# Performance work log

Hardware: AMD Instinct MI355X
Metric: run time of the kernel (lower is better)

## Reference

```python
import jax, jax.numpy as jnp
import numpy as np

N_NODES = 50000
N_EDGES = 800000
N_FEAT = 128
DIM = 64
N_GRAPHS = 512


def setup_inputs() -> dict:
    key = jax.random.key(0)
    k1, k2, k3, k4, k5, k6 = jax.random.split(key, 6)
    x = jax.random.normal(k1, (N_NODES, N_FEAT), dtype=jnp.float32)
    edge_index = jax.random.randint(k2, (2, N_EDGES), 0, N_NODES, dtype=jnp.int64)
    batch = jnp.sort(jax.random.randint(k3, (N_NODES,), 0, N_GRAPHS, dtype=jnp.int64))
    W1 = jax.random.normal(k4, (N_FEAT, DIM), dtype=jnp.float32) * 0.05
    W2 = jax.random.normal(k5, (DIM, DIM), dtype=jnp.float32) * 0.05
    Wfc = jax.random.normal(k6, (DIM, 1), dtype=jnp.float32) * 0.05
    return {"x": x, "edge_index": edge_index, "batch": batch,
            "W1": W1, "W2": W2, "Wfc": Wfc}


def _gcn_conv(h, src, dst, W):
    # GCNConv(normalize=False, bias=False): linear transform then scatter-add
    # over edges: out[dst] += (h @ W)[src]
    h = jnp.einsum('nf,fd->nd', h, W)
    return jax.ops.segment_sum(h[src], dst, num_segments=N_NODES)


def reference(x, edge_index, batch, W1, W2, Wfc):
    src, dst = edge_index[0], edge_index[1]
    h = jax.nn.relu(_gcn_conv(x, src, dst, W1))          # [N, DIM]
    h = _gcn_conv(h, src, dst, W2)                        # [N, DIM]
    # global_mean_pool over graph ids
    counts = jax.ops.segment_sum(jnp.ones((N_NODES,), h.dtype), batch,
                                 num_segments=N_GRAPHS)   # [G]
    pooled = jax.ops.segment_sum(h, batch, num_segments=N_GRAPHS)
    pooled = pooled / jnp.maximum(counts, 1.0)[:, None]   # [G, DIM]
    return jax.nn.sigmoid(pooled @ Wfc)                   # [G, 1]
```

## Files before the change

kernel.cpp:

```cpp
#include <hip/hip_runtime.h>
#include <cmath>

#define N_NODES 50000
#define N_EDGES 800000
#define N_FEAT 128
#define DIM 64
#define N_GRAPHS 512
#define GGRID ((N_NODES + 63) / 64)
#define NBKT GGRID
#define BH_BLK 256
#define EPB (N_EDGES / BH_BLK)
#define BKT_CAP 2048

__device__ __forceinline__ unsigned short f2bf(float f) {
  union { float f; unsigned int u; } v; v.f = f;
  return (unsigned short)((v.u + 0x7FFFu + ((v.u >> 16) & 1u)) >> 16);
}
__device__ __forceinline__ float bf2f(unsigned short u) {
  union { unsigned int u; float f; } v; v.u = (unsigned int)u << 16;
  return v.f;
}

template<int K>
__device__ __forceinline__ void gemm_body_bf(const float* __restrict__ A,
                                             const float* __restrict__ W,
                                             unsigned short* __restrict__ out,
                                             int M, int row0, int tid,
                                             float* sX, float* sW) {
  const int tx = tid & 15, ty = tid >> 4;
  const int q = tid & 7, r0 = tid >> 3;
  float acc[4][4] = {};

  for (int kb = 0; kb < K; kb += 32) {
    __syncthreads();
    if ((kb & 63) == 0) {
#pragma unroll
      for (int i = 0; i < 16; i++)
        sW[i * 256 + tid] = W[kb * 64 + i * 256 + tid];
    }
#pragma unroll
    for (int rr = 0; rr < 64; rr += 32) {
      int r = r0 + rr;
      int gr = row0 + r;
      float4 v = make_float4(0.f, 0.f, 0.f, 0.f);
      if (gr < M) v = *(const float4*)&A[(size_t)gr * K + kb + q * 4];
      *(float4*)&sX[r * 36 + q * 4] = v;
    }
    __syncthreads();

    const int kw = kb & 63;
#pragma unroll 4
    for (int k = 0; k < 32; k += 4) {
      float4 wv[4];
#pragma unroll
      for (int kk = 0; kk < 4; kk++)
        wv[kk] = *(const float4*)&sW[(kw + k + kk) * 64 + tx * 4];
#pragma unroll
      for (int r = 0; r < 4; r++) {
        float4 xv = *(const float4*)&sX[(ty * 4 + r) * 36 + k];
        const float xs[4] = {xv.x, xv.y, xv.z, xv.w};
#pragma unroll
        for (int kk = 0; kk < 4; kk++) {
          acc[r][0] += xs[kk] * wv[kk].x;
          acc[r][1] += xs[kk] * wv[kk].y;
          acc[r][2] += xs[kk] * wv[kk].z;
          acc[r][3] += xs[kk] * wv[kk].w;
        }
      }
    }
  }

#pragma unroll
  for (int r = 0; r < 4; r++) {
    int gr = row0 + ty * 4 + r;
    if (gr < M) {
      ushort4 u;
      u.x = f2bf(acc[r][0]); u.y = f2bf(acc[r][1]);
      u.z = f2bf(acc[r][2]); u.w = f2bf(acc[r][3]);
      *(ushort4*)&out[(size_t)gr * 64 + tx * 4] = u;
    }
  }
}

__global__ __launch_bounds__(256) void fused_main(
    const float* __restrict__ x, const float* __restrict__ W1,
    unsigned short* __restrict__ h1, const int* __restrict__ src,
    const int* __restrict__ dst, int* __restrict__ gcur,
    unsigned int* __restrict__ ebuf, const float* __restrict__ W2,
    const float* __restrict__ Wfc, float* __restrict__ w2fc) {
  __shared__ float sX[64 * 36];
  __shared__ float sW[64 * 64];
  const int tid = threadIdx.x;
  if (blockIdx.x < BH_BLK) {
    int* lh = (int*)sX;
    int* lbase = (int*)sW;
    int* lcur = lbase + NBKT;
    for (int i = tid; i < NBKT; i += 256) { lh[i] = 0; lcur[i] = 0; }
    __syncthreads();
    const int base = blockIdx.x * EPB;
    for (int j = tid; j < EPB; j += 256)
      atomicAdd(&lh[dst[base + j] >> 6], 1);
    __syncthreads();
    for (int i = tid; i < NBKT; i += 256) {
      int n = lh[i];
      lbase[i] = (n > 0) ? i * BKT_CAP + atomicAdd(&gcur[i], n) : 0;
    }
    __syncthreads();
    for (int j = tid; j < EPB; j += 256) {
      int e = base + j;
      int d = dst[e];
      int b = d >> 6;
      int pos = atomicAdd(&lcur[b], 1);
      unsigned int gpos = (unsigned int)(lbase[b] + pos);
      if (gpos < (unsigned int)((b + 1) * BKT_CAP))
        ebuf[gpos] = ((unsigned int)src[e] << 6) | (unsigned int)(d & 63);
    }
  } else if (blockIdx.x == BH_BLK) {
    int k = tid;
    if (k < 64) {
      float s = 0.f;
#pragma unroll 8
      for (int j = 0; j < 64; j++) s += W2[k * 64 + j] * Wfc[j];
      w2fc[k] = s;
    }
  } else {
    gemm_body_bf<N_FEAT>(x, W1, h1, N_NODES, (blockIdx.x - BH_BLK - 1) * 64,
                         tid, sX, sW);
  }
}

__global__ __launch_bounds__(1024, 8) void gather_z_fused(
    const unsigned short* __restrict__ h1,
    const unsigned int* __restrict__ ebuf,
    const int* __restrict__ gcur,
    const float* __restrict__ w2fc,
    float* __restrict__ z) {
  __shared__ unsigned int eL[BKT_CAP];
  __shared__ int colL[BKT_CAP];
  __shared__ int lstart[64];
  __shared__ int lcur[64];
  __shared__ float sw[64];
  const int tid = threadIdx.x;
  const int b = blockIdx.x;
  const int p0 = b * BKT_CAP;
  int cnt = gcur[b];
  if (cnt > BKT_CAP) cnt = BKT_CAP;

  if (tid < 64) { lstart[tid] = 0; sw[tid] = w2fc[tid]; }
  __syncthreads();
  for (int i = tid; i < cnt; i += 1024) {
    unsigned int u = ebuf[p0 + i];
    eL[i] = u;
    atomicAdd(&lstart[u & 63], 1);
  }
  __syncthreads();
  if (tid < 64) {
    int v = lstart[tid], s = v;
#pragma unroll
    for (int off = 1; off < 64; off <<= 1) {
      int t = __shfl_up(s, off, 64);
      if (tid >= off) s += t;
    }
    lstart[tid] = s - v;
    lcur[tid] = s - v;
  }
  __syncthreads();
  for (int i = tid; i < cnt; i += 1024) {
    unsigned int u = eL[i];
    int pos = atomicAdd(&lcur[u & 63], 1);
    colL[pos] = (int)(u >> 6);
  }
  __syncthreads();

  const int lane = tid & 63, w = tid >> 6;
  const int eo = lane >> 4, qfo = (lane & 15) << 2;
#pragma unroll
  for (int ni = 0; ni < 4; ni++) {
    const int r = ni * 16 + w;
    const int i1 = lcur[r];
    int i = lstart[r];
    float4 acc = make_float4(0.f, 0.f, 0.f, 0.f);
    for (; i + 16 <= i1; i += 16) {
      int s0 = colL[i + eo];
      int s1 = colL[i + 4 + eo];
      int s2 = colL[i + 8 + eo];
      int s3 = colL[i + 12 + eo];
      ushort4 u0 = *(const ushort4*)&h1[(size_t)s0 * 64 + qfo];
      ushort4 u1 = *(const ushort4*)&h1[(size_t)s1 * 64 + qfo];
      ushort4 u2 = *(const ushort4*)&h1[(size_t)s2 * 64 + qfo];
      ushort4 u3 = *(const ushort4*)&h1[(size_t)s3 * 64 + qfo];
      acc.x += (bf2f(u0.x) + bf2f(u1.x)) + (bf2f(u2.x) + bf2f(u3.x));
      acc.y += (bf2f(u0.y) + bf2f(u1.y)) + (bf2f(u2.y) + bf2f(u3.y));
      acc.z += (bf2f(u0.z) + bf2f(u1.z)) + (bf2f(u2.z) + bf2f(u3.z));
      acc.w += (bf2f(u0.w) + bf2f(u1.w)) + (bf2f(u2.w) + bf2f(u3.w));
    }
    for (; i + 4 <= i1; i += 4) {
      int s = colL[i + eo];
      ushort4 u = *(const ushort4*)&h1[(size_t)s * 64 + qfo];
      acc.x += bf2f(u.x); acc.y += bf2f(u.y);
      acc.z += bf2f(u.z); acc.w += bf2f(u.w);
    }
    if (eo < i1 - i) {
      int s = colL[i + eo];
      ushort4 u = *(const ushort4*)&h1[(size_t)s * 64 + qfo];
      acc.x += bf2f(u.x); acc.y += bf2f(u.y);
      acc.z += bf2f(u.z); acc.w += bf2f(u.w);
    }
#pragma unroll
    for (int m = 16; m <= 32; m <<= 1) {
      acc.x += __shfl_xor(acc.x, m, 64);
      acc.y += __shfl_xor(acc.y, m, 64);
      acc.z += __shfl_xor(acc.z, m, 64);
      acc.w += __shfl_xor(acc.w, m, 64);
    }
    float p = fmaxf(acc.x, 0.f) * sw[qfo] + fmaxf(acc.y, 0.f) * sw[qfo + 1] +
              fmaxf(acc.z, 0.f) * sw[qfo + 2] + fmaxf(acc.w, 0.f) * sw[qfo + 3];
#pragma unroll
    for (int m = 1; m <= 8; m <<= 1) p += __shfl_xor(p, m, 64);
    int node = b * 64 + r;
    if (lane == 0 && node < N_NODES) z[node] = p;
  }
}

__global__ __launch_bounds__(256) void graph_pool(const float* __restrict__ z,
                                                  const unsigned int* __restrict__ ebuf,
                                                  const int* __restrict__ gcur,
                                                  const int* __restrict__ batch,
                                                  float* __restrict__ out) {
  __shared__ float sacc[4];
  int g = blockIdx.x;
  int tid = threadIdx.x, lane = tid & 63, w = tid >> 6;

  int lo = 0, hi = N_NODES;
  while (lo < hi) { int mid = (lo + hi) >> 1; if (batch[mid] < g) lo = mid + 1; else hi = mid; }
  const int start = lo;
  hi = N_NODES;
  while (lo < hi) { int mid = (lo + hi) >> 1; if (batch[mid] < g + 1) lo = mid + 1; else hi = mid; }
  const int end = lo;

  float s = 0.f;
  if (end > start) {
    const int b0 = start >> 6, b1 = ((end - 1) >> 6) + 1;
    for (int b = b0; b < b1; b++) {
      int bc = gcur[b];
      if (bc > BKT_CAP) bc = BKT_CAP;
      const int q0 = b * BKT_CAP, q1 = q0 + bc;
      const int base = b << 6;
      for (int i = q0 + tid; i < q1; i += 256) {
        unsigned int u = ebuf[i];
        int d = base + (int)(u & 63);
        if (d >= start && d < end) s += z[u >> 6];
      }
    }
  }
#pragma unroll
  for (int off = 32; off; off >>= 1) s += __shfl_down(s, off, 64);
  if (lane == 0) sacc[w] = s;
  __syncthreads();
  if (tid == 0) {
    float v = sacc[0] + sacc[1] + sacc[2] + sacc[3];
    v /= fmaxf((float)(end - start), 1.f);
    out[g] = 1.f / (1.f + expf(-v));
  }
}

extern "C" void kernel_launch(void* const* d_in, const int* in_sizes, int n_in,
                              void* d_out, int out_size, void* d_ws, size_t ws_size,
                              hipStream_t stream) {
  const float* x     = (const float*)d_in[0];
  const int*   ei    = (const int*)d_in[1];
  const int*   batch = (const int*)d_in[2];
  const float* W1    = (const float*)d_in[3];
  const float* W2    = (const float*)d_in[4];
  const float* Wfc   = (const float*)d_in[5];
  float*       out   = (float*)d_out;

  const int* src = ei;
  const int* dst = ei + N_EDGES;

  char* ws = (char*)d_ws;
  unsigned short* h1 = (unsigned short*)(ws);
  float* z    = (float*)(ws + (size_t)N_NODES * DIM * 2);
  float* w2fc = z + N_NODES;
  int*   gcur = (int*)(w2fc + 64);
  unsigned int* ebuf = (unsigned int*)(gcur + 800);

  hipMemsetAsync(gcur, 0, NBKT * sizeof(int), stream);
  fused_main<<<BH_BLK + 1 + GGRID, 256, 0, stream>>>(x, W1, h1, src, dst,
                                                     gcur, ebuf, W2, Wfc, w2fc);

  gather_z_fused<<<NBKT, 1024, 0, stream>>>(h1, ebuf, gcur, w2fc, z);

  graph_pool<<<N_GRAPHS, 256, 0, stream>>>(z, ebuf, gcur, batch, out);
}
```

Before: 138.6 us.

## Compute first GEMM with split-bf16 MFMA and fold memset into a W1 split kernel

Replaces the scalar FP32 shared-memory GEMM for x@W1 with bf16 MFMA 16x16x32 instructions. It keeps near-fp32 accuracy by splitting each operand into high and low bf16 halves and doing three MFMAs per tile. W1 is pre-split and transposed by a new small init kernel, which also zeroes the bucket counters and so replaces the memset. The x tile is converted to bf16 hi/lo on load into an XOR-swizzled LDS layout. The cost is an extra launch, more LDS (32KB per block), and B operands read directly from global memory.

```diff
diff --git a/kernel.cpp b/kernel.cpp
--- a/kernel.cpp
+++ b/kernel.cpp
@@ -12,6 +12,9 @@
 #define EPB (N_EDGES / BH_BLK)
 #define BKT_CAP 2048
 
+typedef short short8 __attribute__((ext_vector_type(8)));
+typedef float floatx4 __attribute__((ext_vector_type(4)));
+
 __device__ __forceinline__ unsigned short f2bf(float f) {
   union { float f; unsigned int u; } v; v.f = f;
   return (unsigned short)((v.u + 0x7FFFu + ((v.u >> 16) & 1u)) >> 16);
@@ -21,80 +24,99 @@
   return v.f;
 }
 
-template<int K>
-__device__ __forceinline__ void gemm_body_bf(const float* __restrict__ A,
-                                             const float* __restrict__ W,
-                                             unsigned short* __restrict__ out,
-                                             int M, int row0, int tid,
-                                             float* sX, float* sW) {
-  const int tx = tid & 15, ty = tid >> 4;
-  const int q = tid & 7, r0 = tid >> 3;
-  float acc[4][4] = {};
-
-  for (int kb = 0; kb < K; kb += 32) {
-    __syncthreads();
-    if ((kb & 63) == 0) {
-#pragma unroll
-      for (int i = 0; i < 16; i++)
-        sW[i * 256 + tid] = W[kb * 64 + i * 256 + tid];
-    }
-#pragma unroll
-    for (int rr = 0; rr < 64; rr += 32) {
-      int r = r0 + rr;
-      int gr = row0 + r;
-      float4 v = make_float4(0.f, 0.f, 0.f, 0.f);
-      if (gr < M) v = *(const float4*)&A[(size_t)gr * K + kb + q * 4];
-      *(float4*)&sX[r * 36 + q * 4] = v;
-    }
-    __syncthreads();
-
-    const int kw = kb & 63;
-#pragma unroll 4
-    for (int k = 0; k < 32; k += 4) {
-      float4 wv[4];
-#pragma unroll
-      for (int kk = 0; kk < 4; kk++)
-        wv[kk] = *(const float4*)&sW[(kw + k + kk) * 64 + tx * 4];
-#pragma unroll
-      for (int r = 0; r < 4; r++) {
-        float4 xv = *(const float4*)&sX[(ty * 4 + r) * 36 + k];
-        const float xs[4] = {xv.x, xv.y, xv.z, xv.w};
-#pragma unroll
-        for (int kk = 0; kk < 4; kk++) {
-          acc[r][0] += xs[kk] * wv[kk].x;
-          acc[r][1] += xs[kk] * wv[kk].y;
-          acc[r][2] += xs[kk] * wv[kk].z;
-          acc[r][3] += xs[kk] * wv[kk].w;
-        }
-      }
-    }
-  }
-
-#pragma unroll
-  for (int r = 0; r < 4; r++) {
-    int gr = row0 + ty * 4 + r;
-    if (gr < M) {
-      ushort4 u;
-      u.x = f2bf(acc[r][0]); u.y = f2bf(acc[r][1]);
-      u.z = f2bf(acc[r][2]); u.w = f2bf(acc[r][3]);
-      *(ushort4*)&out[(size_t)gr * 64 + tx * 4] = u;
+__global__ __launch_bounds__(256) void init_split(const float* __restrict__ W1,
+                                                  unsigned short* __restrict__ w1sh,
+                                                  unsigned short* __restrict__ w1sl,
+                                                  int* __restrict__ gcur) {
+  const int tid = threadIdx.x;
+  if (blockIdx.x == 0) {
+    for (int i = tid; i < NBKT; i += 256) gcur[i] = 0;
+  } else {
+    int idx = (blockIdx.x - 1) * 256 + tid;
+    int kk = idx & 127, c = idx >> 7;
+    float f = W1[kk * 64 + c];
+    unsigned short h = f2bf(f);
+    unsigned short l = f2bf(f - bf2f(h));
+    w1sh[idx] = h;
+    w1sl[idx] = l;
+  }
+}
+
+__device__ __forceinline__ void gemm1_mfma(const float* __restrict__ x,
+                                           const unsigned short* __restrict__ w1sh,
+                                           const unsigned short* __restrict__ w1sl,
+                                           unsigned short* __restrict__ h1,
+                                           int row0, int tid,
+                                           unsigned short* sXh,
+                                           unsigned short* sXl) {
+#pragma unroll
+  for (int i = 0; i < 8; i++) {
+    int fid = i * 256 + tid;
+    int r = fid >> 5;
+    int c4 = (fid & 31) << 2;
+    int gr = row0 + r;
+    float4 v = make_float4(0.f, 0.f, 0.f, 0.f);
+    if (gr < N_NODES) v = *(const float4*)&x[(size_t)gr * N_FEAT + c4];
+    ushort4 h, l;
+    h.x = f2bf(v.x); l.x = f2bf(v.x - bf2f(h.x));
+    h.y = f2bf(v.y); l.y = f2bf(v.y - bf2f(h.y));
+    h.z = f2bf(v.z); l.z = f2bf(v.z - bf2f(h.z));
+    h.w = f2bf(v.w); l.w = f2bf(v.w - bf2f(h.w));
+    int idx = r * 128 + (c4 ^ ((r & 15) << 3));
+    *(ushort4*)&sXh[idx] = h;
+    *(ushort4*)&sXl[idx] = l;
+  }
+  __syncthreads();
+
+  const int lane = tid & 63, w = tid >> 6;
+  const int g = lane >> 4, c15 = lane & 15;
+  const int ra = (w << 4) + c15;
+  const int akey = c15 << 3;
+  floatx4 acc[4];
+#pragma unroll
+  for (int i = 0; i < 4; i++) acc[i] = (floatx4){0.f, 0.f, 0.f, 0.f};
+
+#pragma unroll
+  for (int kb = 0; kb < 128; kb += 32) {
+    const int ka = kb + g * 8;
+    short8 ah = *(const short8*)&sXh[ra * 128 + (ka ^ akey)];
+    short8 al = *(const short8*)&sXl[ra * 128 + (ka ^ akey)];
+#pragma unroll
+    for (int ct = 0; ct < 4; ct++) {
+      const int cb = ct * 16 + c15;
+      short8 bh = *(const short8*)&w1sh[cb * 128 + ka];
+      short8 bl = *(const short8*)&w1sl[cb * 128 + ka];
+      acc[ct] = __builtin_amdgcn_mfma_f32_16x16x32_bf16(ah, bh, acc[ct], 0, 0, 0);
+      acc[ct] = __builtin_amdgcn_mfma_f32_16x16x32_bf16(ah, bl, acc[ct], 0, 0, 0);
+      acc[ct] = __builtin_amdgcn_mfma_f32_16x16x32_bf16(al, bh, acc[ct], 0, 0, 0);
+    }
+  }
+
+#pragma unroll
+  for (int ct = 0; ct < 4; ct++) {
+#pragma unroll
+    for (int r = 0; r < 4; r++) {
+      int gr = row0 + (w << 4) + (g << 2) + r;
+      if (gr < N_NODES) h1[(size_t)gr * 64 + ct * 16 + c15] = f2bf(acc[ct][r]);
     }
   }
 }
 
 __global__ __launch_bounds__(256) void fused_main(
-    const float* __restrict__ x, const float* __restrict__ W1,
+    const float* __restrict__ x,
+    const unsigned short* __restrict__ w1sh,
+    const unsigned short* __restrict__ w1sl,
     unsigned short* __restrict__ h1, const int* __restrict__ src,
     const int* __restrict__ dst, int* __restrict__ gcur,
     unsigned int* __restrict__ ebuf, const float* __restrict__ W2,
     const float* __restrict__ Wfc, float* __restrict__ w2fc) {
-  __shared__ float sX[64 * 36];
-  __shared__ float sW[64 * 64];
+  __shared__ __align__(16) unsigned short sXh[64 * 128];
+  __shared__ __align__(16) unsigned short sXl[64 * 128];
   const int tid = threadIdx.x;
   if (blockIdx.x < BH_BLK) {
-    int* lh = (int*)sX;
-    int* lbase = (int*)sW;
-    int* lcur = lbase + NBKT;
+    int* lh = (int*)sXh;
+    int* lbase = lh + NBKT;
+    int* lcur = (int*)sXl;
     for (int i = tid; i < NBKT; i += 256) { lh[i] = 0; lcur[i] = 0; }
     __syncthreads();
     const int base = blockIdx.x * EPB;
@@ -124,8 +146,8 @@
       w2fc[k] = s;
     }
   } else {
-    gemm_body_bf<N_FEAT>(x, W1, h1, N_NODES, (blockIdx.x - BH_BLK - 1) * 64,
-                         tid, sX, sW);
+    gemm1_mfma(x, w1sh, w1sl, h1, (blockIdx.x - BH_BLK - 1) * 64, tid,
+               sXh, sXl);
   }
 }
 
@@ -282,12 +304,16 @@
   unsigned short* h1 = (unsigned short*)(ws);
   float* z    = (float*)(ws + (size_t)N_NODES * DIM * 2);
   float* w2fc = z + N_NODES;
-  int*   gcur = (int*)(w2fc + 64);
+  unsigned short* w1sh = (unsigned short*)(w2fc + 64);
+  unsigned short* w1sl = w1sh + N_FEAT * DIM;
+  int*   gcur = (int*)(w1sl + N_FEAT * DIM);
   unsigned int* ebuf = (unsigned int*)(gcur + 800);
 
-  hipMemsetAsync(gcur, 0, NBKT * sizeof(int), stream);
-  fused_main<<<BH_BLK + 1 + GGRID, 256, 0, stream>>>(x, W1, h1, src, dst,
-                                                     gcur, ebuf, W2, Wfc, w2fc);
+  init_split<<<33, 256, 0, stream>>>(W1, w1sh, w1sl, gcur);
+
+  fused_main<<<BH_BLK + 1 + GGRID, 256, 0, stream>>>(x, w1sh, w1sl, h1, src,
+                                                     dst, gcur, ebuf, W2, Wfc,
+                                                     w2fc);
 
   gather_z_fused<<<NBKT, 1024, 0, stream>>>(h1, ebuf, gcur, w2fc, z);
 
```

New measurement: 141.0 us. No clear change (+1.7%).
